# Performance work log

Measured on AMD Instinct MI355X. Metric: run time of the kernel, lower is better.

Reference implementation:

```python
import jax, jax.numpy as jnp
import numpy as np
from jax import lax

INPUT_SIZE = 32
HIDDEN = 64
BATCH = 8192
SEQ = 128


def _lstm_layer(x, w_ih, w_hh, b_ih, b_hh):
    """Single unidirectional LSTM layer, PyTorch gate order (i, f, g, o).
    x: [B, T, D] -> (outputs [B, T, H], final h [B, H])"""
    B = x.shape[0]
    H = w_hh.shape[1]
    # Precompute input contributions for all timesteps: [B, T, 4H]
    xg = jnp.einsum('btd,gd->btg', x, w_ih) + b_ih + b_hh

    def step(carry, xg_t):
        h, c = carry
        gates = xg_t + h @ w_hh.T  # [B, 4H]
        i, f, g, o = jnp.split(gates, 4, axis=-1)
        i = jax.nn.sigmoid(i)
        f = jax.nn.sigmoid(f)
        g = jnp.tanh(g)
        o = jax.nn.sigmoid(o)
        c = f * c + i * g
        h = o * jnp.tanh(c)
        return (h, c), h

    h0 = jnp.zeros((B, H), dtype=x.dtype)
    c0 = jnp.zeros((B, H), dtype=x.dtype)
    (h_n, _), hs = lax.scan(step, (h0, c0), jnp.swapaxes(xg, 0, 1))
    return jnp.swapaxes(hs, 0, 1), h_n


def setup_inputs() -> dict:
    key = jax.random.key(0)
    ks = jax.random.split(key, 12)
    H4 = 4 * HIDDEN
    s_ih0 = 1.0 / np.sqrt(INPUT_SIZE)
    s_h = 1.0 / np.sqrt(HIDDEN)
    x = jax.random.normal(ks[0], (BATCH, SEQ, INPUT_SIZE), dtype=jnp.float32)
    # Biases: zeros with forget-gate bias = 1 (per _init_weights)
    b = jnp.zeros((H4,), dtype=jnp.float32).at[HIDDEN:2 * HIDDEN].set(1.0)
    return {
        'x': x,
        'w_ih0': jax.random.uniform(ks[1], (H4, INPUT_SIZE), jnp.float32, -s_ih0, s_ih0),
        'w_hh0': jax.random.uniform(ks[2], (H4, HIDDEN), jnp.float32, -s_h, s_h),
        'b_ih0': b,
        'b_hh0': jnp.zeros((H4,), dtype=jnp.float32),
        'w_ih1': jax.random.uniform(ks[3], (H4, HIDDEN), jnp.float32, -s_h, s_h),
        'w_hh1': jax.random.uniform(ks[4], (H4, HIDDEN), jnp.float32, -s_h, s_h),
        'b_ih1': b,
        'b_hh1': jnp.zeros((H4,), dtype=jnp.float32),
        'fc_w': jax.random.uniform(ks[5], (1, HIDDEN), jnp.float32, -s_h, s_h),
        'fc_b': jnp.zeros((1,), dtype=jnp.float32),
    }


def reference(x, w_ih0, w_hh0, b_ih0, b_hh0, w_ih1, w_hh1, b_ih1, b_hh1, fc_w, fc_b):
    # 2-layer LSTM (inter-layer dropout is identity at inference)
    h1_seq, _ = _lstm_layer(x, w_ih0, w_hh0, b_ih0, b_hh0)
    _, h_final = _lstm_layer(h1_seq, w_ih1, w_hh1, b_ih1, b_hh1)
    # dropout(h_final) is identity in eval mode; final linear head -> squeeze
    logit = h_final @ fc_w.T + fc_b  # [B, 1]
    return logit.squeeze(-1)  # [B]
```

## Files before the change

kernel.cpp:

```cpp
#include <hip/hip_runtime.h>


#define TT  128
#define DIN 32
#define BT  16
#define L2E 1.44269504088896340736f

typedef _Float16 h8 __attribute__((ext_vector_type(8)));
typedef __fp16   p2 __attribute__((ext_vector_type(2)));
typedef float    f4 __attribute__((ext_vector_type(4)));

__device__ __forceinline__ h8 cvt8s(const float* p, float s) {
    float4 a = *(const float4*)p;
    float4 b = *(const float4*)(p + 4);
    union { h8 v; p2 q[4]; } u;
    u.q[0] = __builtin_amdgcn_cvt_pkrtz(a.x * s, a.y * s);
    u.q[1] = __builtin_amdgcn_cvt_pkrtz(a.z * s, a.w * s);
    u.q[2] = __builtin_amdgcn_cvt_pkrtz(b.x * s, b.y * s);
    u.q[3] = __builtin_amdgcn_cvt_pkrtz(b.z * s, b.w * s);
    return u.v;
}
__device__ __forceinline__ h8 cvt8(const float* p) {
    float4 a = *(const float4*)p;
    float4 b = *(const float4*)(p + 4);
    union { h8 v; p2 q[4]; } u;
    u.q[0] = __builtin_amdgcn_cvt_pkrtz(a.x, a.y);
    u.q[1] = __builtin_amdgcn_cvt_pkrtz(a.z, a.w);
    u.q[2] = __builtin_amdgcn_cvt_pkrtz(b.x, b.y);
    u.q[3] = __builtin_amdgcn_cvt_pkrtz(b.z, b.w);
    return u.v;
}

__device__ __forceinline__ float elem(const f4& acc, float& c) {
    float Ei = __builtin_amdgcn_exp2f(-acc[0]);
    float Ef = __builtin_amdgcn_exp2f(-acc[1]);
    float Eg = __builtin_amdgcn_exp2f(-acc[2]);
    float Eo = __builtin_amdgcn_exp2f(-acc[3]);
    float a = 1.f + Ei, b = 1.f + Eg, d = 1.f + Ef;
    float P = a * b;
    float N = c * P + (1.f - Eg) * d;
    c = N * __builtin_amdgcn_rcpf(P * d);
    float Ec = __builtin_amdgcn_exp2f(-2.f * L2E * c);
    return (1.f - Ec) * __builtin_amdgcn_rcpf((1.f + Ec) * (1.f + Eo));
}

__global__ __launch_bounds__(512, 4)
void lstm2_fused(const float* __restrict__ x,
                 const float* __restrict__ wih0, const float* __restrict__ whh0,
                 const float* __restrict__ bih0, const float* __restrict__ bhh0,
                 const float* __restrict__ wih1, const float* __restrict__ whh1,
                 const float* __restrict__ bih1, const float* __restrict__ bhh1,
                 const float* __restrict__ fcw,  const float* __restrict__ fcb,
                 float* __restrict__ out)
{
    const int tid  = threadIdx.x;
    const int lane = tid & 63;
    const int wv   = tid >> 6;
    const int bl   = lane & 15;
    const int kg   = lane >> 4;

    __shared__ alignas(16) unsigned short hb[2][2][BT * 64];
    __shared__ float wpart[8][BT];

    for (int i = tid; i < (int)(sizeof(hb) / 4); i += 512) ((int*)hb)[i] = 0;

    h8 W0[2][3], W1[2][4];
    f4 b0v[2], b1v[2];
    #pragma unroll
    for (int t = 0; t < 2; ++t) {
        const int hbse = 8 * wv + 4 * t;
        const int gam  = bl & 3;
        const int g    = 64 * gam + hbse + (bl >> 2);
        const float sc = (gam == 2) ? 2.f * L2E : L2E;
        W0[t][0] = cvt8s(wih0 + g * 32 + 8 * kg, sc);
        W0[t][1] = cvt8s(whh0 + g * 64 + 8 * kg, sc);
        W0[t][2] = cvt8s(whh0 + g * 64 + 32 + 8 * kg, sc);
        W1[t][0] = cvt8s(wih1 + g * 64 + 8 * kg, sc);
        W1[t][1] = cvt8s(wih1 + g * 64 + 32 + 8 * kg, sc);
        W1[t][2] = cvt8s(whh1 + g * 64 + 8 * kg, sc);
        W1[t][3] = cvt8s(whh1 + g * 64 + 32 + 8 * kg, sc);
        #pragma unroll
        for (int r = 0; r < 4; ++r) {
            const int gr = 64 * r + hbse + kg;
            const float scr = (r == 2) ? 2.f * L2E : L2E;
            b0v[t][r] = (bih0[gr] + bhh0[gr]) * scr;
            b1v[t][r] = (bih1[gr] + bhh1[gr]) * scr;
        }
    }

    const int bbase = blockIdx.x * BT;
    const float* xp = x + (size_t)(bbase + bl) * (TT * DIN) + 8 * kg;

    float c0[2] = {0.f, 0.f}, c1[2] = {0.f, 0.f}, h1f[2] = {0.f, 0.f};

    __syncthreads();

    const int swz = (bl & 7) << 4;
    char* lb = (char*)hb;
    const int rowoff = bl * 128;
    const int rd0 = rowoff + ((16 * kg) ^ swz);
    const int rd1 = rowoff + ((64 + 16 * kg) ^ swz);
    const int wro0 = rowoff + ((16 * wv + 2 * kg) ^ swz);
    const int wro1 = rowoff + ((16 * wv + 8 + 2 * kg) ^ swz);

    auto L0 = [&](const h8& xc, const h8& hr0, const h8& hr1, int wp) {
        #pragma unroll
        for (int t = 0; t < 2; ++t) {
            f4 acc = b0v[t];
            acc = __builtin_amdgcn_mfma_f32_16x16x32_f16(W0[t][1], hr0, acc, 0, 0, 0);
            acc = __builtin_amdgcn_mfma_f32_16x16x32_f16(W0[t][2], hr1, acc, 0, 0, 0);
            acc = __builtin_amdgcn_mfma_f32_16x16x32_f16(W0[t][0], xc,  acc, 0, 0, 0);
            float h = elem(acc, c0[t]);
            *(_Float16*)(lb + wp * 2048 + (t ? wro1 : wro0)) = (_Float16)h;
        }
    };

    auto L1 = [&](const h8& g0a, const h8& g0b, const h8& g1a, const h8& g1b,
                  int wp, bool store) {
        #pragma unroll
        for (int t = 0; t < 2; ++t) {
            f4 acc = b1v[t];
            acc = __builtin_amdgcn_mfma_f32_16x16x32_f16(W1[t][0], g0a, acc, 0, 0, 0);
            acc = __builtin_amdgcn_mfma_f32_16x16x32_f16(W1[t][1], g0b, acc, 0, 0, 0);
            acc = __builtin_amdgcn_mfma_f32_16x16x32_f16(W1[t][2], g1a, acc, 0, 0, 0);
            acc = __builtin_amdgcn_mfma_f32_16x16x32_f16(W1[t][3], g1b, acc, 0, 0, 0);
            float h = elem(acc, c1[t]);
            h1f[t] = h;
            if (store) *(_Float16*)(lb + 4096 + wp * 2048 + (t ? wro1 : wro0)) = (_Float16)h;
        }
    };

    {
        h8 xc  = cvt8(xp);
        h8 hr0 = *(const h8*)(lb + 2048 + rd0);
        h8 hr1 = *(const h8*)(lb + 2048 + rd1);
        L0(xc, hr0, hr1, 0);
        __syncthreads();
    }

    for (int it = 1; it < TT; ++it) {
        const int wp = it & 1, rp = wp ^ 1;
        h8 xc  = cvt8(xp + it * DIN);
        h8 hr0 = *(const h8*)(lb + rp * 2048 + rd0);
        h8 hr1 = *(const h8*)(lb + rp * 2048 + rd1);
        h8 g1a = *(const h8*)(lb + 4096 + rp * 2048 + rd0);
        h8 g1b = *(const h8*)(lb + 4096 + rp * 2048 + rd1);
        L0(xc, hr0, hr1, wp);
        L1(hr0, hr1, g1a, g1b, wp, true);
        __syncthreads();
    }

    {
        const int rp = 1;
        h8 hr0 = *(const h8*)(lb + rp * 2048 + rd0);
        h8 hr1 = *(const h8*)(lb + rp * 2048 + rd1);
        h8 g1a = *(const h8*)(lb + 4096 + rp * 2048 + rd0);
        h8 g1b = *(const h8*)(lb + 4096 + rp * 2048 + rd1);
        L1(hr0, hr1, g1a, g1b, 0, false);
    }

    float part = h1f[0] * fcw[8 * wv + kg] + h1f[1] * fcw[8 * wv + 4 + kg];
    part += __shfl_xor(part, 16, 64);
    part += __shfl_xor(part, 32, 64);
    if (lane < 16) wpart[wv][lane] = part;
    __syncthreads();
    if (tid < BT) {
        float s = fcb[0];
        #pragma unroll
        for (int w = 0; w < 8; ++w) s += wpart[w][tid];
        out[bbase + tid] = s;
    }
}

extern "C" void kernel_launch(void* const* d_in, const int* in_sizes, int n_in,
                              void* d_out, int out_size, void* d_ws, size_t ws_size,
                              hipStream_t stream) {
    (void)in_sizes; (void)n_in; (void)d_ws; (void)ws_size; (void)out_size;
    lstm2_fused<<<dim3(8192 / BT), dim3(512), 0, stream>>>(
        (const float*)d_in[0],
        (const float*)d_in[1], (const float*)d_in[2],
        (const float*)d_in[3], (const float*)d_in[4],
        (const float*)d_in[5], (const float*)d_in[6],
        (const float*)d_in[7], (const float*)d_in[8],
        (const float*)d_in[9], (const float*)d_in[10],
        (float*)d_out);
}
```

Before: 184.8 us.

## Double threads per block so each wave owns one gate tile per layer

Doubles the block from 512 to 1024 threads (16 waves), so each wave computes a single 16-row gate tile per layer instead of two, halving per-thread weight registers and the serial MFMA+elementwise chain per step. Biases move from registers to LDS and are reloaded each step to cut register pressure further. The cost is more waves joining each per-timestep __syncthreads barrier, extra LDS reads per step, and a tighter launch-bounds occupancy target that could force register spilling.

```diff
diff --git a/kernel.cpp b/kernel.cpp
--- a/kernel.cpp
+++ b/kernel.cpp
@@ -44,7 +44,7 @@
     return (1.f - Ec) * __builtin_amdgcn_rcpf((1.f + Ec) * (1.f + Eo));
 }
 
-__global__ __launch_bounds__(512, 4)
+__global__ __launch_bounds__(1024, 8)
 void lstm2_fused(const float* __restrict__ x,
                  const float* __restrict__ wih0, const float* __restrict__ whh0,
                  const float* __restrict__ bih0, const float* __restrict__ bhh0,
@@ -60,74 +60,74 @@
     const int kg   = lane >> 4;
 
     __shared__ alignas(16) unsigned short hb[2][2][BT * 64];
-    __shared__ float wpart[8][BT];
+    __shared__ alignas(16) float blds[2][64][4];
+    __shared__ float wpart[16][BT];
 
-    for (int i = tid; i < (int)(sizeof(hb) / 4); i += 512) ((int*)hb)[i] = 0;
+    for (int i = tid; i < (int)(sizeof(hb) / 4); i += 1024) ((int*)hb)[i] = 0;
 
-    h8 W0[2][3], W1[2][4];
-    f4 b0v[2], b1v[2];
-    #pragma unroll
-    for (int t = 0; t < 2; ++t) {
-        const int hbse = 8 * wv + 4 * t;
-        const int gam  = bl & 3;
-        const int g    = 64 * gam + hbse + (bl >> 2);
-        const float sc = (gam == 2) ? 2.f * L2E : L2E;
-        W0[t][0] = cvt8s(wih0 + g * 32 + 8 * kg, sc);
-        W0[t][1] = cvt8s(whh0 + g * 64 + 8 * kg, sc);
-        W0[t][2] = cvt8s(whh0 + g * 64 + 32 + 8 * kg, sc);
-        W1[t][0] = cvt8s(wih1 + g * 64 + 8 * kg, sc);
-        W1[t][1] = cvt8s(wih1 + g * 64 + 32 + 8 * kg, sc);
-        W1[t][2] = cvt8s(whh1 + g * 64 + 8 * kg, sc);
-        W1[t][3] = cvt8s(whh1 + g * 64 + 32 + 8 * kg, sc);
+    if (tid < 128) {
+        const int layer = tid >> 6, idx = tid & 63;
+        const int wvv = idx >> 2, kgg = idx & 3;
+        const float* bi = layer ? bih1 : bih0;
+        const float* bh = layer ? bhh1 : bhh0;
         #pragma unroll
         for (int r = 0; r < 4; ++r) {
-            const int gr = 64 * r + hbse + kg;
+            const int gr = 64 * r + 4 * wvv + kgg;
             const float scr = (r == 2) ? 2.f * L2E : L2E;
-            b0v[t][r] = (bih0[gr] + bhh0[gr]) * scr;
-            b1v[t][r] = (bih1[gr] + bhh1[gr]) * scr;
+            blds[layer][idx][r] = (bi[gr] + bh[gr]) * scr;
         }
+    }
+
+    h8 W0[3], W1[4];
+    {
+        const int gam = bl & 3;
+        const int g   = 64 * gam + 4 * wv + (bl >> 2);
+        const float sc = (gam == 2) ? 2.f * L2E : L2E;
+        W0[0] = cvt8s(wih0 + g * 32 + 8 * kg, sc);
+        W0[1] = cvt8s(whh0 + g * 64 + 8 * kg, sc);
+        W0[2] = cvt8s(whh0 + g * 64 + 32 + 8 * kg, sc);
+        W1[0] = cvt8s(wih1 + g * 64 + 8 * kg, sc);
+        W1[1] = cvt8s(wih1 + g * 64 + 32 + 8 * kg, sc);
+        W1[2] = cvt8s(whh1 + g * 64 + 8 * kg, sc);
+        W1[3] = cvt8s(whh1 + g * 64 + 32 + 8 * kg, sc);
     }
 
     const int bbase = blockIdx.x * BT;
     const float* xp = x + (size_t)(bbase + bl) * (TT * DIN) + 8 * kg;
 
-    float c0[2] = {0.f, 0.f}, c1[2] = {0.f, 0.f}, h1f[2] = {0.f, 0.f};
-
-    __syncthreads();
+    float c0 = 0.f, c1 = 0.f, h1f = 0.f;
 
     const int swz = (bl & 7) << 4;
     char* lb = (char*)hb;
     const int rowoff = bl * 128;
     const int rd0 = rowoff + ((16 * kg) ^ swz);
     const int rd1 = rowoff + ((64 + 16 * kg) ^ swz);
-    const int wro0 = rowoff + ((16 * wv + 2 * kg) ^ swz);
-    const int wro1 = rowoff + ((16 * wv + 8 + 2 * kg) ^ swz);
+    const int wro = rowoff + ((8 * wv + 2 * kg) ^ swz);
+
+    __syncthreads();
+
+    const f4* bp0 = (const f4*)blds[0][4 * wv + kg];
+    const f4* bp1 = (const f4*)blds[1][4 * wv + kg];
 
     auto L0 = [&](const h8& xc, const h8& hr0, const h8& hr1, int wp) {
-        #pragma unroll
-        for (int t = 0; t < 2; ++t) {
-            f4 acc = b0v[t];
-            acc = __builtin_amdgcn_mfma_f32_16x16x32_f16(W0[t][1], hr0, acc, 0, 0, 0);
-            acc = __builtin_amdgcn_mfma_f32_16x16x32_f16(W0[t][2], hr1, acc, 0, 0, 0);
-            acc = __builtin_amdgcn_mfma_f32_16x16x32_f16(W0[t][0], xc,  acc, 0, 0, 0);
-            float h = elem(acc, c0[t]);
-            *(_Float16*)(lb + wp * 2048 + (t ? wro1 : wro0)) = (_Float16)h;
-        }
+        f4 acc = *bp0;
+        acc = __builtin_amdgcn_mfma_f32_16x16x32_f16(W0[1], hr0, acc, 0, 0, 0);
+        acc = __builtin_amdgcn_mfma_f32_16x16x32_f16(W0[2], hr1, acc, 0, 0, 0);
+        acc = __builtin_amdgcn_mfma_f32_16x16x32_f16(W0[0], xc,  acc, 0, 0, 0);
+        float h = elem(acc, c0);
+        *(_Float16*)(lb + wp * 2048 + wro) = (_Float16)h;
     };
 
-    auto L1 = [&](const h8& g0a, const h8& g0b, const h8& g1a, const h8& g1b,
+    auto L1 = [&](const h8& hr0, const h8& hr1, const h8& g1a, const h8& g1b,
                   int wp, bool store) {
-        #pragma unroll
-        for (int t = 0; t < 2; ++t) {
-            f4 acc = b1v[t];
-            acc = __builtin_amdgcn_mfma_f32_16x16x32_f16(W1[t][0], g0a, acc, 0, 0, 0);
-            acc = __builtin_amdgcn_mfma_f32_16x16x32_f16(W1[t][1], g0b, acc, 0, 0, 0);
-            acc = __builtin_amdgcn_mfma_f32_16x16x32_f16(W1[t][2], g1a, acc, 0, 0, 0);
-            acc = __builtin_amdgcn_mfma_f32_16x16x32_f16(W1[t][3], g1b, acc, 0, 0, 0);
-            float h = elem(acc, c1[t]);
-            h1f[t] = h;
-            if (store) *(_Float16*)(lb + 4096 + wp * 2048 + (t ? wro1 : wro0)) = (_Float16)h;
-        }
+        f4 acc = *bp1;
+        acc = __builtin_amdgcn_mfma_f32_16x16x32_f16(W1[0], hr0, acc, 0, 0, 0);
+        acc = __builtin_amdgcn_mfma_f32_16x16x32_f16(W1[1], hr1, acc, 0, 0, 0);
+        acc = __builtin_amdgcn_mfma_f32_16x16x32_f16(W1[2], g1a, acc, 0, 0, 0);
+        acc = __builtin_amdgcn_mfma_f32_16x16x32_f16(W1[3], g1b, acc, 0, 0, 0);
+        float h = elem(acc, c1);
+        h1f = h;
+        if (store) *(_Float16*)(lb + 4096 + wp * 2048 + wro) = (_Float16)h;
     };
 
     {
@@ -159,7 +159,7 @@
         L1(hr0, hr1, g1a, g1b, 0, false);
     }
 
-    float part = h1f[0] * fcw[8 * wv + kg] + h1f[1] * fcw[8 * wv + 4 + kg];
+    float part = h1f * fcw[4 * wv + kg];
     part += __shfl_xor(part, 16, 64);
     part += __shfl_xor(part, 32, 64);
     if (lane < 16) wpart[wv][lane] = part;
@@ -167,7 +167,7 @@
     if (tid < BT) {
         float s = fcb[0];
         #pragma unroll
-        for (int w = 0; w < 8; ++w) s += wpart[w][tid];
+        for (int w = 0; w < 16; ++w) s += wpart[w][tid];
         out[bbase + tid] = s;
     }
 }
@@ -176,7 +176,7 @@
                               void* d_out, int out_size, void* d_ws, size_t ws_size,
                               hipStream_t stream) {
     (void)in_sizes; (void)n_in; (void)d_ws; (void)ws_size; (void)out_size;
-    lstm2_fused<<<dim3(8192 / BT), dim3(512), 0, stream>>>(
+    lstm2_fused<<<dim3(8192 / BT), dim3(1024), 0, stream>>>(
         (const float*)d_in[0],
         (const float*)d_in[1], (const float*)d_in[2],
         (const float*)d_in[3], (const float*)d_in[4],
```

New measurement: 265.3 us. 43.6% more time.

## Interleave two batch sub-tiles per block to overlap MFMA with gate math

Applied to the files above, without the earlier changes.

Each block now handles 32 batch rows as two independent 16-row sub-tiles, A and B. Each half-step runs the MFMAs of one sub-tile while computing the elementwise gate updates of the other, so matrix and transcendental work can overlap, and the next step's x values are loaded one step ahead. The grid is halved and launch bounds drop to 2 blocks per SM, which gives more registers per thread but fewer resident blocks. Barriers per timestep double, and the grid of 256 blocks may leave some compute units underused.

```diff
diff --git a/kernel.cpp b/kernel.cpp
--- a/kernel.cpp
+++ b/kernel.cpp
@@ -3,12 +3,13 @@
 
 #define TT  128
 #define DIN 32
-#define BT  16
 #define L2E 1.44269504088896340736f
 
 typedef _Float16 h8 __attribute__((ext_vector_type(8)));
 typedef __fp16   p2 __attribute__((ext_vector_type(2)));
 typedef float    f4 __attribute__((ext_vector_type(4)));
+
+#define MFMA(A, B, C) __builtin_amdgcn_mfma_f32_16x16x32_f16((A), (B), (C), 0, 0, 0)
 
 __device__ __forceinline__ h8 cvt8s(const float* p, float s) {
     float4 a = *(const float4*)p;
@@ -20,9 +21,8 @@
     u.q[3] = __builtin_amdgcn_cvt_pkrtz(b.z * s, b.w * s);
     return u.v;
 }
-__device__ __forceinline__ h8 cvt8(const float* p) {
-    float4 a = *(const float4*)p;
-    float4 b = *(const float4*)(p + 4);
+
+__device__ __forceinline__ h8 pack8(const float4& a, const float4& b) {
     union { h8 v; p2 q[4]; } u;
     u.q[0] = __builtin_amdgcn_cvt_pkrtz(a.x, a.y);
     u.q[1] = __builtin_amdgcn_cvt_pkrtz(a.z, a.w);
@@ -44,7 +44,7 @@
     return (1.f - Ec) * __builtin_amdgcn_rcpf((1.f + Ec) * (1.f + Eo));
 }
 
-__global__ __launch_bounds__(512, 4)
+__global__ __launch_bounds__(512, 2)
 void lstm2_fused(const float* __restrict__ x,
                  const float* __restrict__ wih0, const float* __restrict__ whh0,
                  const float* __restrict__ bih0, const float* __restrict__ bhh0,
@@ -59,116 +59,227 @@
     const int bl   = lane & 15;
     const int kg   = lane >> 4;
 
-    __shared__ alignas(16) unsigned short hb[2][2][BT * 64];
-    __shared__ float wpart[8][BT];
+    __shared__ alignas(16) unsigned short hb[2][2][2][16 * 64];
+    __shared__ float wpart[2][8][16];
 
     for (int i = tid; i < (int)(sizeof(hb) / 4); i += 512) ((int*)hb)[i] = 0;
 
     h8 W0[2][3], W1[2][4];
     f4 b0v[2], b1v[2];
     #pragma unroll
-    for (int t = 0; t < 2; ++t) {
-        const int hbse = 8 * wv + 4 * t;
+    for (int k = 0; k < 2; ++k) {
+        const int hbse = 8 * wv + 4 * k;
         const int gam  = bl & 3;
         const int g    = 64 * gam + hbse + (bl >> 2);
         const float sc = (gam == 2) ? 2.f * L2E : L2E;
-        W0[t][0] = cvt8s(wih0 + g * 32 + 8 * kg, sc);
-        W0[t][1] = cvt8s(whh0 + g * 64 + 8 * kg, sc);
-        W0[t][2] = cvt8s(whh0 + g * 64 + 32 + 8 * kg, sc);
-        W1[t][0] = cvt8s(wih1 + g * 64 + 8 * kg, sc);
-        W1[t][1] = cvt8s(wih1 + g * 64 + 32 + 8 * kg, sc);
-        W1[t][2] = cvt8s(whh1 + g * 64 + 8 * kg, sc);
-        W1[t][3] = cvt8s(whh1 + g * 64 + 32 + 8 * kg, sc);
+        W0[k][0] = cvt8s(wih0 + g * 32 + 8 * kg, sc);
+        W0[k][1] = cvt8s(whh0 + g * 64 + 8 * kg, sc);
+        W0[k][2] = cvt8s(whh0 + g * 64 + 32 + 8 * kg, sc);
+        W1[k][0] = cvt8s(wih1 + g * 64 + 8 * kg, sc);
+        W1[k][1] = cvt8s(wih1 + g * 64 + 32 + 8 * kg, sc);
+        W1[k][2] = cvt8s(whh1 + g * 64 + 8 * kg, sc);
+        W1[k][3] = cvt8s(whh1 + g * 64 + 32 + 8 * kg, sc);
         #pragma unroll
         for (int r = 0; r < 4; ++r) {
             const int gr = 64 * r + hbse + kg;
             const float scr = (r == 2) ? 2.f * L2E : L2E;
-            b0v[t][r] = (bih0[gr] + bhh0[gr]) * scr;
-            b1v[t][r] = (bih1[gr] + bhh1[gr]) * scr;
-        }
-    }
-
-    const int bbase = blockIdx.x * BT;
-    const float* xp = x + (size_t)(bbase + bl) * (TT * DIN) + 8 * kg;
-
-    float c0[2] = {0.f, 0.f}, c1[2] = {0.f, 0.f}, h1f[2] = {0.f, 0.f};
-
-    __syncthreads();
+            b0v[k][r] = (bih0[gr] + bhh0[gr]) * scr;
+            b1v[k][r] = (bih1[gr] + bhh1[gr]) * scr;
+        }
+    }
+
+    const int bbase = blockIdx.x * 32;
+    const float* xpA = x + (size_t)(bbase + bl) * (TT * DIN) + 8 * kg;
+    const float* xpB = xpA + 16 * (TT * DIN);
+
+    float c0A[2] = {0.f, 0.f}, c1A[2] = {0.f, 0.f};
+    float c0B[2] = {0.f, 0.f}, c1B[2] = {0.f, 0.f};
+    f4 a0A[2], a1A[2], a0B[2], a1B[2];
+    float h1fA[2], h1fB[2];
 
     const int swz = (bl & 7) << 4;
     char* lb = (char*)hb;
     const int rowoff = bl * 128;
-    const int rd0 = rowoff + ((16 * kg) ^ swz);
-    const int rd1 = rowoff + ((64 + 16 * kg) ^ swz);
+    const int rd0  = rowoff + ((16 * kg) ^ swz);
+    const int rd1  = rowoff + ((64 + 16 * kg) ^ swz);
     const int wro0 = rowoff + ((16 * wv + 2 * kg) ^ swz);
     const int wro1 = rowoff + ((16 * wv + 8 + 2 * kg) ^ swz);
 
-    auto L0 = [&](const h8& xc, const h8& hr0, const h8& hr1, int wp) {
-        #pragma unroll
-        for (int t = 0; t < 2; ++t) {
-            f4 acc = b0v[t];
-            acc = __builtin_amdgcn_mfma_f32_16x16x32_f16(W0[t][1], hr0, acc, 0, 0, 0);
-            acc = __builtin_amdgcn_mfma_f32_16x16x32_f16(W0[t][2], hr1, acc, 0, 0, 0);
-            acc = __builtin_amdgcn_mfma_f32_16x16x32_f16(W0[t][0], xc,  acc, 0, 0, 0);
-            float h = elem(acc, c0[t]);
-            *(_Float16*)(lb + wp * 2048 + (t ? wro1 : wro0)) = (_Float16)h;
-        }
-    };
-
-    auto L1 = [&](const h8& g0a, const h8& g0b, const h8& g1a, const h8& g1b,
-                  int wp, bool store) {
-        #pragma unroll
-        for (int t = 0; t < 2; ++t) {
-            f4 acc = b1v[t];
-            acc = __builtin_amdgcn_mfma_f32_16x16x32_f16(W1[t][0], g0a, acc, 0, 0, 0);
-            acc = __builtin_amdgcn_mfma_f32_16x16x32_f16(W1[t][1], g0b, acc, 0, 0, 0);
-            acc = __builtin_amdgcn_mfma_f32_16x16x32_f16(W1[t][2], g1a, acc, 0, 0, 0);
-            acc = __builtin_amdgcn_mfma_f32_16x16x32_f16(W1[t][3], g1b, acc, 0, 0, 0);
-            float h = elem(acc, c1[t]);
-            h1f[t] = h;
-            if (store) *(_Float16*)(lb + 4096 + wp * 2048 + (t ? wro1 : wro0)) = (_Float16)h;
-        }
-    };
+    __syncthreads();
+
+    h8 xcurA = pack8(*(const float4*)xpA, *(const float4*)(xpA + 4));
+    h8 xcurB = pack8(*(const float4*)xpB, *(const float4*)(xpB + 4));
+
+    for (int t = 0; t < TT; ++t) {
+        const int p_t   = t & 1;
+        const int p_tm1 = (t - 1) & 1;
+
+        {
+            const int tn = (t + 1 < TT) ? t + 1 : TT - 1;
+            float4 xa = *(const float4*)(xpA + tn * DIN);
+            float4 xb = *(const float4*)(xpA + tn * DIN + 4);
+
+            const char* rA0 = lb + 0 * 8192 + 0 * 4096 + p_tm1 * 2048;
+            h8 hr0 = *(const h8*)(rA0 + rd0);
+            h8 hr1 = *(const h8*)(rA0 + rd1);
+            #pragma unroll
+            for (int k = 0; k < 2; ++k) {
+                f4 acc = b0v[k];
+                acc = MFMA(W0[k][1], hr0, acc);
+                acc = MFMA(W0[k][2], hr1, acc);
+                acc = MFMA(W0[k][0], xcurA, acc);
+                a0A[k] = acc;
+            }
+            if (t >= 1) {
+                const char* rA1 = lb + 0 * 8192 + 1 * 4096 + p_t * 2048;
+                h8 g1a = *(const h8*)(rA1 + rd0);
+                h8 g1b = *(const h8*)(rA1 + rd1);
+                #pragma unroll
+                for (int k = 0; k < 2; ++k) {
+                    f4 acc = b1v[k];
+                    acc = MFMA(W1[k][0], hr0, acc);
+                    acc = MFMA(W1[k][1], hr1, acc);
+                    acc = MFMA(W1[k][2], g1a, acc);
+                    acc = MFMA(W1[k][3], g1b, acc);
+                    a1A[k] = acc;
+                }
+            }
+            if (t >= 1) {
+                char* D = lb + 1 * 8192 + 0 * 4096 + p_tm1 * 2048;
+                #pragma unroll
+                for (int k = 0; k < 2; ++k) {
+                    float h = elem(a0B[k], c0B[k]);
+                    *(_Float16*)(D + (k ? wro1 : wro0)) = (_Float16)h;
+                }
+            }
+            if (t >= 2) {
+                char* D = lb + 1 * 8192 + 1 * 4096 + p_t * 2048;
+                #pragma unroll
+                for (int k = 0; k < 2; ++k) {
+                    float h = elem(a1B[k], c1B[k]);
+                    *(_Float16*)(D + (k ? wro1 : wro0)) = (_Float16)h;
+                }
+            }
+            xcurA = pack8(xa, xb);
+            __syncthreads();
+        }
+
+        {
+            const int tn = (t + 1 < TT) ? t + 1 : TT - 1;
+            float4 xa = *(const float4*)(xpB + tn * DIN);
+            float4 xb = *(const float4*)(xpB + tn * DIN + 4);
+
+            const char* rB0 = lb + 1 * 8192 + 0 * 4096 + p_tm1 * 2048;
+            h8 hr0 = *(const h8*)(rB0 + rd0);
+            h8 hr1 = *(const h8*)(rB0 + rd1);
+            #pragma unroll
+            for (int k = 0; k < 2; ++k) {
+                f4 acc = b0v[k];
+                acc = MFMA(W0[k][1], hr0, acc);
+                acc = MFMA(W0[k][2], hr1, acc);
+                acc = MFMA(W0[k][0], xcurB, acc);
+                a0B[k] = acc;
+            }
+            if (t >= 1) {
+                const char* rB1 = lb + 1 * 8192 + 1 * 4096 + p_t * 2048;
+                h8 g1a = *(const h8*)(rB1 + rd0);
+                h8 g1b = *(const h8*)(rB1 + rd1);
+                #pragma unroll
+                for (int k = 0; k < 2; ++k) {
+                    f4 acc = b1v[k];
+                    acc = MFMA(W1[k][0], hr0, acc);
+                    acc = MFMA(W1[k][1], hr1, acc);
+                    acc = MFMA(W1[k][2], g1a, acc);
+                    acc = MFMA(W1[k][3], g1b, acc);
+                    a1B[k] = acc;
+                }
+            }
+            {
+                char* D = lb + 0 * 8192 + 0 * 4096 + p_t * 2048;
+                #pragma unroll
+                for (int k = 0; k < 2; ++k) {
+                    float h = elem(a0A[k], c0A[k]);
+                    *(_Float16*)(D + (k ? wro1 : wro0)) = (_Float16)h;
+                }
+            }
+            if (t >= 1) {
+                char* D = lb + 0 * 8192 + 1 * 4096 + p_tm1 * 2048;
+                #pragma unroll
+                for (int k = 0; k < 2; ++k) {
+                    float h = elem(a1A[k], c1A[k]);
+                    *(_Float16*)(D + (k ? wro1 : wro0)) = (_Float16)h;
+                }
+            }
+            xcurB = pack8(xa, xb);
+            __syncthreads();
+        }
+    }
 
     {
-        h8 xc  = cvt8(xp);
-        h8 hr0 = *(const h8*)(lb + 2048 + rd0);
-        h8 hr1 = *(const h8*)(lb + 2048 + rd1);
-        L0(xc, hr0, hr1, 0);
+        const char* rA0 = lb + 0 * 8192 + 0 * 4096 + 1 * 2048;
+        h8 hr0 = *(const h8*)(rA0 + rd0);
+        h8 hr1 = *(const h8*)(rA0 + rd1);
+        const char* rA1 = lb + 0 * 8192 + 1 * 4096 + 0 * 2048;
+        h8 g1a = *(const h8*)(rA1 + rd0);
+        h8 g1b = *(const h8*)(rA1 + rd1);
+        #pragma unroll
+        for (int k = 0; k < 2; ++k) {
+            f4 acc = b1v[k];
+            acc = MFMA(W1[k][0], hr0, acc);
+            acc = MFMA(W1[k][1], hr1, acc);
+            acc = MFMA(W1[k][2], g1a, acc);
+            acc = MFMA(W1[k][3], g1b, acc);
+            a1A[k] = acc;
+        }
+        char* D0 = lb + 1 * 8192 + 0 * 4096 + 1 * 2048;
+        char* D1 = lb + 1 * 8192 + 1 * 4096 + 0 * 2048;
+        #pragma unroll
+        for (int k = 0; k < 2; ++k) {
+            float h0 = elem(a0B[k], c0B[k]);
+            *(_Float16*)(D0 + (k ? wro1 : wro0)) = (_Float16)h0;
+            float h1 = elem(a1B[k], c1B[k]);
+            *(_Float16*)(D1 + (k ? wro1 : wro0)) = (_Float16)h1;
+        }
         __syncthreads();
     }
-
-    for (int it = 1; it < TT; ++it) {
-        const int wp = it & 1, rp = wp ^ 1;
-        h8 xc  = cvt8(xp + it * DIN);
-        h8 hr0 = *(const h8*)(lb + rp * 2048 + rd0);
-        h8 hr1 = *(const h8*)(lb + rp * 2048 + rd1);
-        h8 g1a = *(const h8*)(lb + 4096 + rp * 2048 + rd0);
-        h8 g1b = *(const h8*)(lb + 4096 + rp * 2048 + rd1);
-        L0(xc, hr0, hr1, wp);
-        L1(hr0, hr1, g1a, g1b, wp, true);
-        __syncthreads();
-    }
-
     {
-        const int rp = 1;
-        h8 hr0 = *(const h8*)(lb + rp * 2048 + rd0);
-        h8 hr1 = *(const h8*)(lb + rp * 2048 + rd1);
-        h8 g1a = *(const h8*)(lb + 4096 + rp * 2048 + rd0);
-        h8 g1b = *(const h8*)(lb + 4096 + rp * 2048 + rd1);
-        L1(hr0, hr1, g1a, g1b, 0, false);
-    }
-
-    float part = h1f[0] * fcw[8 * wv + kg] + h1f[1] * fcw[8 * wv + 4 + kg];
-    part += __shfl_xor(part, 16, 64);
-    part += __shfl_xor(part, 32, 64);
-    if (lane < 16) wpart[wv][lane] = part;
+        const char* rB0 = lb + 1 * 8192 + 0 * 4096 + 1 * 2048;
+        h8 hr0 = *(const h8*)(rB0 + rd0);
+        h8 hr1 = *(const h8*)(rB0 + rd1);
+        const char* rB1 = lb + 1 * 8192 + 1 * 4096 + 0 * 2048;
+        h8 g1a = *(const h8*)(rB1 + rd0);
+        h8 g1b = *(const h8*)(rB1 + rd1);
+        #pragma unroll
+        for (int k = 0; k < 2; ++k) {
+            f4 acc = b1v[k];
+            acc = MFMA(W1[k][0], hr0, acc);
+            acc = MFMA(W1[k][1], hr1, acc);
+            acc = MFMA(W1[k][2], g1a, acc);
+            acc = MFMA(W1[k][3], g1b, acc);
+            a1B[k] = acc;
+        }
+        #pragma unroll
+        for (int k = 0; k < 2; ++k) h1fA[k] = elem(a1A[k], c1A[k]);
+    }
+    #pragma unroll
+    for (int k = 0; k < 2; ++k) h1fB[k] = elem(a1B[k], c1B[k]);
+
+    const float fw0 = fcw[8 * wv + kg];
+    const float fw1 = fcw[8 * wv + 4 + kg];
+    float pA = h1fA[0] * fw0 + h1fA[1] * fw1;
+    float pB = h1fB[0] * fw0 + h1fB[1] * fw1;
+    pA += __shfl_xor(pA, 16, 64);
+    pA += __shfl_xor(pA, 32, 64);
+    pB += __shfl_xor(pB, 16, 64);
+    pB += __shfl_xor(pB, 32, 64);
+    if (lane < 16) { wpart[0][wv][lane] = pA; wpart[1][wv][lane] = pB; }
     __syncthreads();
-    if (tid < BT) {
-        float s = fcb[0];
-        #pragma unroll
-        for (int w = 0; w < 8; ++w) s += wpart[w][tid];
-        out[bbase + tid] = s;
+    if (tid < 32) {
+        const int s = tid >> 4, b = tid & 15;
+        float sum = fcb[0];
+        #pragma unroll
+        for (int w = 0; w < 8; ++w) sum += wpart[s][w][b];
+        out[bbase + s * 16 + b] = sum;
     }
 }
 
@@ -176,7 +287,7 @@
                               void* d_out, int out_size, void* d_ws, size_t ws_size,
                               hipStream_t stream) {
     (void)in_sizes; (void)n_in; (void)d_ws; (void)ws_size; (void)out_size;
-    lstm2_fused<<<dim3(8192 / BT), dim3(512), 0, stream>>>(
+    lstm2_fused<<<dim3(8192 / 32), dim3(512), 0, stream>>>(
         (const float*)d_in[0],
         (const float*)d_in[1], (const float*)d_in[2],
         (const float*)d_in[3], (const float*)d_in[4],
```

New measurement: 225.6 us. +22.1%, slower.
